# Kernel tuning notes

Hardware: AMD Instinct MI355X
Metric: run time of the kernel (lower is better)

The kernel has to match this reference:

```python
import jax, jax.numpy as jnp
import numpy as np

B, S, V, D, E, L = 4, 256, 50000, 300, 128, 20  # batch, seq, vocab, embed, encoder_size, labels


def _gru(x, h0, wih, whh, bih, bhh):
    """Unidirectional torch-style GRU. x: [B,S,Din], h0: [B,H]. Returns ([B,S,H], [B,H])."""
    gx = jnp.einsum('bsd,hd->bsh', x, wih) + bih  # precompute all input projections [B,S,3H]

    def step(h, gx_t):
        gh = h @ whh.T + bhh
        xr, xz, xn = jnp.split(gx_t, 3, axis=-1)
        hr, hz, hn = jnp.split(gh, 3, axis=-1)
        r = jax.nn.sigmoid(xr + hr)
        z = jax.nn.sigmoid(xz + hz)
        n = jnp.tanh(xn + r * hn)
        h2 = (1.0 - z) * n + z * h
        return h2, h2

    hT, hs = jax.lax.scan(step, h0, jnp.swapaxes(gx, 0, 1))
    return jnp.swapaxes(hs, 0, 1), hT


def _bigru(x, h0, pf, pb):
    """Bidirectional GRU. h0: [2,B,H]. Returns ([B,S,2H], [2,B,H])."""
    of, hf = _gru(x, h0[0], *pf)
    ob, hb = _gru(x[:, ::-1], h0[1], *pb)
    return jnp.concatenate([of, ob[:, ::-1]], axis=-1), jnp.stack([hf, hb])


def reference(inputs, emb,
              enc_wih_f, enc_whh_f, enc_bih_f, enc_bhh_f,
              enc_wih_b, enc_whh_b, enc_bih_b, enc_bhh_b,
              hid_wih_f, hid_whh_f, hid_bih_f, hid_bhh_f,
              hid_wih_b, hid_whh_b, hid_bih_b, hid_bhh_b,
              agg_wih_f, agg_whh_f, agg_bih_f, agg_bhh_f,
              agg_wih_b, agg_whh_b, agg_bih_b, agg_bhh_b,
              Wc1, Wc2, vc, Wb, Wd, vd, Wm, vm, Ws, vs, Wp, vp, Wpred):
    x = emb[inputs]                                # [B,S,D]
    b = x.shape[0]
    h0 = jnp.zeros((2, b, E), x.dtype)
    hp, hidden = _bigru(x, h0,
                        (enc_wih_f, enc_whh_f, enc_bih_f, enc_bhh_f),
                        (enc_wih_b, enc_whh_b, enc_bih_b, enc_bhh_b))   # [B,S,2E]
    hq, _ = _bigru(hp, hidden,
                   (hid_wih_f, hid_whh_f, hid_bih_f, hid_bhh_f),
                   (hid_wih_b, hid_whh_b, hid_bih_b, hid_bhh_b))        # [B,S,2E]

    # ptc: additive attention, score = vc . tanh(Wc1 hp_k + Wc2 hq_q)
    s1 = jnp.einsum('bkd,ed->bke', hp, Wc1)
    s2 = jnp.einsum('bqd,ed->bqe', hq, Wc2)
    sc = jnp.einsum('bqke,e->bqk', jnp.tanh(s1[:, None] + s2[:, :, None]), vc)
    ptc = jnp.einsum('bqk,bkd->bqd', jax.nn.softmax(sc, -1), hp)

    # ptb: bilinear attention, score = hq_q . (Wb hp_k)
    sc = jnp.einsum('bqd,bkd->bqk', hq, jnp.einsum('bkd,ed->bke', hp, Wb))
    ptb = jnp.einsum('bqk,bkd->bqd', jax.nn.softmax(sc, -1), hp)

    # ptd: score = vd . tanh(Wd (hp_k * hq_q))
    sc = jnp.einsum('bqke,e->bqk', jnp.tanh(jnp.einsum('bqkd,ed->bqke', hp[:, None] * hq[:, :, None], Wd)), vd)
    ptd = jnp.einsum('bqk,bkd->bqd', jax.nn.softmax(sc, -1), hp)

    # ptm: score = vm . tanh(Wm (hp_k - hq_q))
    sc = jnp.einsum('bqke,e->bqk', jnp.tanh(jnp.einsum('bqkd,ed->bqke', hp[:, None] - hq[:, :, None], Wm)), vm)
    ptm = jnp.einsum('bqk,bkd->bqd', jax.nn.softmax(sc, -1), hp)

    # pts: self, score = vs . tanh(Ws (hq_k * hq_q))
    sc = jnp.einsum('bqke,e->bqk', jnp.tanh(jnp.einsum('bqkd,ed->bqke', hq[:, None] * hq[:, :, None], Ws)), vs)
    pts = jnp.einsum('bqk,bkd->bqd', jax.nn.softmax(sc, -1), hq)

    agg = jnp.concatenate([hq, pts, ptc, ptd, ptb, ptm], axis=-1)  # [B,S,12E]
    agg_rep, _ = _bigru(agg, jnp.zeros((2, b, E), x.dtype),
                        (agg_wih_f, agg_whh_f, agg_bih_f, agg_bhh_f),
                        (agg_wih_b, agg_whh_b, agg_bih_b, agg_bhh_b))  # [B,S,2E]

    # pooled query rl over hq
    sj = jnp.einsum('bse,e->bs', jnp.tanh(jnp.einsum('bsd,ed->bse', hq, Wp)), vp)
    rl = jnp.einsum('bs,bsd->bd', jax.nn.softmax(sj, -1), hq)       # [B,2E]

    # final pooling over agg_rep (note: no tanh here, matching source)
    sc = jnp.einsum('bse,e->bs',
                    jnp.einsum('bsd,ed->bse', agg_rep, Wc1) + jnp.einsum('bd,ed->be', rl, Wc2)[:, None],
                    vc)
    rr = jnp.einsum('bs,bsd->bd', jax.nn.softmax(sc, -1), agg_rep)  # [B,2E]
    return jax.nn.sigmoid(rr @ Wpred.T)                              # [B,labels]


def setup_inputs() -> dict:
    key = jax.random.key(0)
    ks = iter(jax.random.split(key, 64))
    f = lambda *s: jax.random.normal(next(ks), s, jnp.float32) * 0.05
    H3 = 3 * E
    return dict(
        inputs=jax.random.randint(next(ks), (B, S), 0, V),
        emb=f(V, D),
        enc_wih_f=f(H3, D), enc_whh_f=f(H3, E), enc_bih_f=f(H3), enc_bhh_f=f(H3),
        enc_wih_b=f(H3, D), enc_whh_b=f(H3, E), enc_bih_b=f(H3), enc_bhh_b=f(H3),
        hid_wih_f=f(H3, 2 * E), hid_whh_f=f(H3, E), hid_bih_f=f(H3), hid_bhh_f=f(H3),
        hid_wih_b=f(H3, 2 * E), hid_whh_b=f(H3, E), hid_bih_b=f(H3), hid_bhh_b=f(H3),
        agg_wih_f=f(H3, 12 * E), agg_whh_f=f(H3, E), agg_bih_f=f(H3), agg_bhh_f=f(H3),
        agg_wih_b=f(H3, 12 * E), agg_whh_b=f(H3, E), agg_bih_b=f(H3), agg_bhh_b=f(H3),
        Wc1=f(E, 2 * E), Wc2=f(E, 2 * E), vc=f(E),
        Wb=f(2 * E, 2 * E),
        Wd=f(E, 2 * E), vd=f(E),
        Wm=f(E, 2 * E), vm=f(E),
        Ws=f(E, 2 * E), vs=f(E),
        Wp=f(E, 2 * E), vp=f(E),
        Wpred=f(L, 2 * E),
    )
```

## Files before the change

### kernel.cpp

```cpp
#include <hip/hip_runtime.h>
#include <math.h>

#define BB 4
#define SS 256
#define DD 300
#define DP 304
#define EE 128
#define LL 20
#define H3 384
#define D2 256
#define D12 1536

typedef __attribute__((ext_vector_type(8)))  short short8;
typedef __attribute__((ext_vector_type(16))) float f32x16;
typedef __attribute__((ext_vector_type(2)))  float f32x2;

__device__ __forceinline__ float tanh_fast(float x){
  float e = __expf(2.f*x);
  return 1.f - 2.f/(e+1.f);
}
__device__ __forceinline__ float sigmoidf_(float x){ return 1.f/(1.f+__expf(-x)); }
__device__ __forceinline__ float bf16_to_f(unsigned u){ return __builtin_bit_cast(float, u<<16); }
__device__ __forceinline__ float bf16hi_to_f(unsigned u){ return __builtin_bit_cast(float, u & 0xFFFF0000u); }
__device__ __forceinline__ unsigned bf16_rne(float f){
  unsigned u = __builtin_bit_cast(unsigned, f);
  return (u + 0x7FFFu + ((u>>16)&1u)) >> 16;
}
__device__ __forceinline__ unsigned pack_bf16x2(float lo, float hi){
  return bf16_rne(lo) | (bf16_rne(hi)<<16);
}

__global__ void k_cvt_bf16(const float* __restrict__ src, unsigned short* __restrict__ dst, int n2){
  int i = blockIdx.x*blockDim.x + threadIdx.x;
  if (i < n2){
    float2 f = *(const float2*)(src + 2*i);
    *(unsigned*)(dst + 2*i) = pack_bf16x2(f.x, f.y);
  }
}

struct CvtSeg { const float* src; unsigned short* dst; int rows, Ks, Kd; };
struct CvtArgs { CvtSeg s[13]; };
__global__ void k_cvt_weights(CvtArgs a){
  CvtSeg sg = a.s[blockIdx.y];
  int p = blockIdx.x*256 + threadIdx.x;
  int Kd2 = sg.Kd>>1;
  int npairs = sg.rows*Kd2;
  if (p >= npairs) return;
  int row = p/Kd2, kk = (p - row*Kd2)*2;
  float f0 = (kk   < sg.Ks)? sg.src[(size_t)row*sg.Ks+kk  ] : 0.f;
  float f1 = (kk+1 < sg.Ks)? sg.src[(size_t)row*sg.Ks+kk+1] : 0.f;
  *(unsigned*)(sg.dst + (size_t)row*sg.Kd + kk) = pack_bf16x2(f0,f1);
}

__global__ void k_embed(const int* __restrict__ inp, const float* __restrict__ emb,
                        unsigned short* __restrict__ xb){
  int row = blockIdx.x;
  int idx = inp[row];
  const float* src = emb + (size_t)idx*DD;
  unsigned short* dst = xb + (size_t)row*DP;
  int p = threadIdx.x;
  if (p < DP/2){
    float f0 = (2*p   < DD)? src[2*p  ] : 0.f;
    float f1 = (2*p+1 < DD)? src[2*p+1] : 0.f;
    *(unsigned*)(dst + 2*p) = pack_bf16x2(f0,f1);
  }
}

__global__ void k_init2(float* __restrict__ gf, const float* __restrict__ bf,
                        float* __restrict__ gb, const float* __restrict__ bb){
  int row = blockIdx.x, n = threadIdx.x;
  gf[(size_t)row*H3+n] = bf[n];
  gb[(size_t)row*H3+n] = bb[n];
}

__global__ __launch_bounds__(64) void k_mmbf(
    const unsigned short* __restrict__ X, const unsigned short* __restrict__ W,
    const float* __restrict__ bias, float* __restrict__ out,
    int N, int K, int kspan){
  int lane=threadIdx.x, col=lane&31, half=lane>>5;
  int n0=blockIdx.x*32, m0=blockIdx.y*64;
  int ks=blockIdx.z*kspan, ke=ks+kspan; if (ke>K) ke=K;
  const unsigned short* pa0 = X + (size_t)(m0+col)*K + half*8;
  const unsigned short* pa1 = pa0 + (size_t)32*K;
  const unsigned short* pb  = W + (size_t)(n0+col)*K + half*8;
  f32x16 acc0={}, acc1={};
  #pragma unroll 2
  for (int k=ks;k<ke;k+=16){
    short8 a0=__builtin_bit_cast(short8, *(const uint4*)(pa0+k));
    short8 a1=__builtin_bit_cast(short8, *(const uint4*)(pa1+k));
    short8 bv=__builtin_bit_cast(short8, *(const uint4*)(pb +k));
    acc0=__builtin_amdgcn_mfma_f32_32x32x16_bf16(a0,bv,acc0,0,0,0);
    acc1=__builtin_amdgcn_mfma_f32_32x32x16_bf16(a1,bv,acc1,0,0,0);
  }
  int cn = n0+col;
  if (gridDim.z==1){
    float bn = bias? bias[cn] : 0.f;
    #pragma unroll
    for (int r=0;r<16;r++){
      int row=(r&3)+8*(r>>2)+4*half;
      out[(size_t)(m0+row)*N+cn]    = acc0[r]+bn;
      out[(size_t)(m0+32+row)*N+cn] = acc1[r]+bn;
    }
  } else {
    #pragma unroll
    for (int r=0;r<16;r++){
      int row=(r&3)+8*(r>>2)+4*half;
      atomicAdd(&out[(size_t)(m0+row)*N+cn],    acc0[r]);
      atomicAdd(&out[(size_t)(m0+32+row)*N+cn], acc1[r]);
    }
  }
}

#define GW 8
#define CH 16
#define PSTR 9

__global__ __launch_bounds__(512, 1) void k_gru_scan(
                          const float* __restrict__ gxf, const float* __restrict__ gxb,
                          const float* __restrict__ whhf, const float* __restrict__ whhb,
                          const float* __restrict__ bhhf, const float* __restrict__ bhhb,
                          const float* __restrict__ h0,
                          float* __restrict__ out,
                          unsigned short* __restrict__ out_bf,
                          float* __restrict__ hT){
  int b=blockIdx.x, dir=blockIdx.y, tid=threadIdx.x;
  const float* gx  = dir? gxb : gxf;
  const float* whh = dir? whhb : whhf;
  const float* bhh = dir? bhhb : bhhf;
  int w = tid>>6, lane = tid&63;
  int chunk = w*CH;

  f32x2 wv[3][CH];
  #pragma unroll
  for (int p=0;p<3;p++){
    const float* r0 = whh + (size_t)(lane+64*(2*p  ))*EE + chunk;
    const float* r1 = whh + (size_t)(lane+64*(2*p+1))*EE + chunk;
    #pragma unroll
    for (int k=0;k<CH;k++){ wv[p][k].x = r0[k]; wv[p][k].y = r1[k]; }
  }

  __shared__ __align__(16) float hsh[EE];
  __shared__ float part[H3*PSTR];

  bool comb = (tid < EE);
  float hprev=0.f, b_r=0.f, b_z=0.f, b_n=0.f;
  float xrA=0.f,xzA=0.f,xnA=0.f, xrB=0.f,xzB=0.f,xnB=0.f;
  if (comb){
    int r = tid;
    b_r = bhh[r]; b_z = bhh[r+EE]; b_n = bhh[r+2*EE];
    hprev = h0? h0[((size_t)dir*BB+b)*EE + r] : 0.f;
    hsh[r] = hprev;
    int s0 = dir? (SS-1) : 0;
    int s1 = dir? (SS-2) : 1;
    const float* g0 = gx + ((size_t)b*SS+s0)*H3;
    const float* g1 = gx + ((size_t)b*SS+s1)*H3;
    xrA=g0[r]; xzA=g0[r+EE]; xnA=g0[r+2*EE];
    xrB=g1[r]; xzB=g1[r+EE]; xnB=g1[r+2*EE];
  }
  __syncthreads();

  auto dotphase = [&](){
    float vh = hsh[chunk + (lane & (CH-1))];
    f32x2 acc0={0.f,0.f}, acc1={0.f,0.f}, acc2={0.f,0.f};
    #pragma unroll
    for (int k=0;k<CH;k++){
      float s = __builtin_bit_cast(float,
                  __builtin_amdgcn_readlane(__builtin_bit_cast(int, vh), k));
      acc0 += wv[0][k]*s;
      acc1 += wv[1][k]*s;
      acc2 += wv[2][k]*s;
    }
    part[(lane      )*PSTR + w] = acc0.x;
    part[(lane+ 64  )*PSTR + w] = acc0.y;
    part[(lane+128  )*PSTR + w] = acc1.x;
    part[(lane+192  )*PSTR + w] = acc1.y;
    part[(lane+256  )*PSTR + w] = acc2.x;
    part[(lane+320  )*PSTR + w] = acc2.y;
  };

  auto combphase = [&](int t, float xr, float xz, float xn,
                       float& pxr, float& pxz, float& pxn){
    int r = tid;
    float ar=0.f, az=0.f, an=0.f;
    #pragma unroll
    for (int c=0;c<GW;c++){
      ar += part[(r      )*PSTR+c];
      az += part[(r+128  )*PSTR+c];
      an += part[(r+256  )*PSTR+c];
    }
    int s = dir? (SS-1-t) : t;
    float rg = sigmoidf_(xr + ar + b_r);
    float zg = sigmoidf_(xz + az + b_z);
    float ng = tanh_fast(xn + rg*(an + b_n));
    float h2 = (1.f-zg)*ng + zg*hprev;
    hprev = h2;
    hsh[r] = h2;
    size_t oi = ((size_t)b*SS+s)*D2 + (size_t)dir*EE + r;
    out[oi] = h2;
    if (out_bf) out_bf[oi] = (unsigned short)bf16_rne(h2);
    if (t+2 < SS){
      int sn = dir? (SS-3-t) : (t+2);
      const float* gn = gx + ((size_t)b*SS+sn)*H3;
      pxr=gn[r]; pxz=gn[r+EE]; pxn=gn[r+2*EE];
    }
  };

  for (int t=0;t<SS;t+=2){
    dotphase();
    __syncthreads();
    if (comb) combphase(t, xrA,xzA,xnA, xrA,xzA,xnA);
    __syncthreads();
    dotphase();
    __syncthreads();
    if (comb) combphase(t+1, xrB,xzB,xnB, xrB,xzB,xnB);
    __syncthreads();
  }
  if (hT && comb) hT[((size_t)dir*BB+b)*EE+tid]=hprev;
}

__global__ void k_copy_hq(const unsigned short* __restrict__ hqb, unsigned short* __restrict__ aggb){
  int row=blockIdx.x;
  aggb[(size_t)row*D12 + threadIdx.x] = hqb[(size_t)row*D2 + threadIdx.x];
}

__device__ __forceinline__ void softmax256(float val, float* red, float* p){
  int tid=threadIdx.x;
  red[tid]=val; __syncthreads();
  for (int st=128; st>0; st>>=1){ if (tid<st) red[tid]=fmaxf(red[tid],red[tid+st]); __syncthreads(); }
  float mx=red[0]; __syncthreads();
  float ex=__expf(val-mx); red[tid]=ex; __syncthreads();
  for (int st=128; st>0; st>>=1){ if (tid<st) red[tid]+=red[tid+st]; __syncthreads(); }
  float inv=1.f/red[0];
  p[tid]=ex*inv; __syncthreads();
}

__global__ __launch_bounds__(256) void k_attn_add(const float* __restrict__ A, const float* __restrict__ Bq,
                          const float* __restrict__ v, float sign,
                          const float* __restrict__ V, unsigned short* __restrict__ aggout, int off){
  __shared__ __align__(16) float bq[EE];
  __shared__ __align__(16) float vv[EE];
  __shared__ float p[SS]; __shared__ float red[SS];
  int q=blockIdx.x, b=blockIdx.y, tid=threadIdx.x;
  if (tid<EE){ bq[tid]=sign*Bq[((size_t)b*SS+q)*EE+tid]; vv[tid]=v[tid]; }
  __syncthreads();
  const float* Ar = A + ((size_t)b*SS+tid)*EE;
  float s=0.f;
  #pragma unroll
  for (int e=0;e<EE;e+=4){
    float4 a=*(const float4*)(Ar+e);
    float4 bb=*(const float4*)(bq+e);
    float4 vw=*(const float4*)(vv+e);
    s += vw.x*tanh_fast(a.x+bb.x)+vw.y*tanh_fast(a.y+bb.y)+vw.z*tanh_fast(a.z+bb.z)+vw.w*tanh_fast(a.w+bb.w);
  }
  softmax256(s, red, p);
  const float* V0 = V + (size_t)b*SS*D2;
  float o=0.f;
  for (int k=0;k<SS;k++) o += p[k]*V0[(size_t)k*D2+tid];
  aggout[((size_t)b*SS+q)*D12 + off + tid] = (unsigned short)bf16_rne(o);
}

__global__ __launch_bounds__(256) void k_attn_bil(const float* __restrict__ Pb, const float* __restrict__ hq,
                          const float* __restrict__ V, unsigned short* __restrict__ aggout, int off){
  __shared__ __align__(16) float hqq[D2];
  __shared__ float p[SS]; __shared__ float red[SS];
  int q=blockIdx.x, b=blockIdx.y, tid=threadIdx.x;
  hqq[tid]=hq[((size_t)b*SS+q)*D2+tid];
  __syncthreads();
  const float* Pr = Pb + ((size_t)b*SS+tid)*D2;
  float s=0.f;
  #pragma unroll
  for (int d=0;d<D2;d+=4){
    float4 a=*(const float4*)(Pr+d);
    float4 hh=*(const float4*)(hqq+d);
    s += a.x*hh.x+a.y*hh.y+a.z*hh.z+a.w*hh.w;
  }
  softmax256(s, red, p);
  const float* V0 = V + (size_t)b*SS*D2;
  float o=0.f;
  for (int k=0;k<SS;k++) o += p[k]*V0[(size_t)k*D2+tid];
  aggout[((size_t)b*SS+q)*D12 + off + tid] = (unsigned short)bf16_rne(o);
}

__global__ __launch_bounds__(256, 2) void k_mulattn_fused(
    const unsigned short* __restrict__ keysb,
    const float* __restrict__ qm,
    const unsigned short* __restrict__ Wb,
    const float* __restrict__ v,
    const float* __restrict__ V,
    unsigned short* __restrict__ aggout, int off){
  __shared__ __align__(16) float qrow[D2];
  __shared__ __align__(16) float vrow[EE];
  __shared__ float scq[SS];
  __shared__ float red[SS];
  __shared__ float p[SS];
  int q=blockIdx.x, b=blockIdx.y, tid=threadIdx.x;
  int wave=tid>>6, lane=tid&63;
  size_t bS = (size_t)b*SS;
  qrow[tid]=qm[(bS+q)*D2+tid];
  if (tid<EE) vrow[tid]=v[tid];
  __syncthreads();

  f32x16 acc[2][4]={};
  int m0 = wave*64;
  int col = lane&31, half = lane>>5;
  const unsigned short* krow0 = keysb + (bS + m0 + col)*D2 + half*8;
  const unsigned short* krow1 = krow0 + 32*D2;
  const unsigned short* wrow[4];
  #pragma unroll
  for (int n=0;n<4;n++) wrow[n] = Wb + (size_t)(n*32+col)*D2 + half*8;

  for (int d0=0; d0<D2; d0+=16){
    float4 qsA = *(const float4*)&qrow[d0 + half*8];
    float4 qsB = *(const float4*)&qrow[d0 + half*8 + 4];
    short8 bfrag[4];
    #pragma unroll
    for (int n=0;n<4;n++) bfrag[n] = __builtin_bit_cast(short8, *(const uint4*)(wrow[n]+d0));
    #pragma unroll
    for (int i=0;i<2;i++){
      uint4 raw = *(const uint4*)((i? krow1:krow0) + d0);
      float f0=bf16_to_f(raw.x)*qsA.x, f1=bf16hi_to_f(raw.x)*qsA.y;
      float f2=bf16_to_f(raw.y)*qsA.z, f3=bf16hi_to_f(raw.y)*qsA.w;
      float f4=bf16_to_f(raw.z)*qsB.x, f5=bf16hi_to_f(raw.z)*qsB.y;
      float f6=bf16_to_f(raw.w)*qsB.z, f7=bf16hi_to_f(raw.w)*qsB.w;
      uint4 pk;
      pk.x=pack_bf16x2(f0,f1);
      pk.y=pack_bf16x2(f2,f3);
      pk.z=pack_bf16x2(f4,f5);
      pk.w=pack_bf16x2(f6,f7);
      short8 afrag = __builtin_bit_cast(short8, pk);
      #pragma unroll
      for (int n=0;n<4;n++)
        acc[i][n] = __builtin_amdgcn_mfma_f32_32x32x16_bf16(afrag, bfrag[n], acc[i][n], 0,0,0);
    }
  }
  float vn[4];
  #pragma unroll
  for (int n=0;n<4;n++) vn[n]=vrow[n*32+col];
  #pragma unroll
  for (int i=0;i<2;i++){
    #pragma unroll
    for (int r=0;r<16;r++){
      float s = vn[0]*tanh_fast(acc[i][0][r]) + vn[1]*tanh_fast(acc[i][1][r])
              + vn[2]*tanh_fast(acc[i][2][r]) + vn[3]*tanh_fast(acc[i][3][r]);
      s += __shfl_xor(s,1,32); s += __shfl_xor(s,2,32); s += __shfl_xor(s,4,32);
      s += __shfl_xor(s,8,32); s += __shfl_xor(s,16,32);
      int k = m0 + i*32 + (r&3) + 8*(r>>2) + 4*half;
      scq[k] = s;
    }
  }
  __syncthreads();
  float val = scq[tid];
  softmax256(val, red, p);
  const float* V0 = V + bS*D2;
  float o=0.f;
  for (int k=0;k<SS;k++) o += p[k]*V0[(size_t)k*D2+tid];
  aggout[(bS+q)*D12 + off + tid] = (unsigned short)bf16_rne(o);
}

__global__ __launch_bounds__(256) void k_rl(const float* __restrict__ spj, const float* __restrict__ hq,
                    const float* __restrict__ vp, const float* __restrict__ Wc2,
                    float* __restrict__ sB){
  __shared__ __align__(16) float vpl[EE];
  __shared__ float p[SS]; __shared__ float red[SS];
  __shared__ __align__(16) float rr[D2];
  int b=blockIdx.x, tid=threadIdx.x;
  if (tid<EE) vpl[tid]=vp[tid];
  __syncthreads();
  const float* row = spj + ((size_t)b*SS+tid)*EE;
  float sj=0.f;
  #pragma unroll
  for (int e=0;e<EE;e+=4){
    float4 a=*(const float4*)(row+e);
    float4 vw=*(const float4*)(vpl+e);
    sj += vw.x*tanh_fast(a.x)+vw.y*tanh_fast(a.y)+vw.z*tanh_fast(a.z)+vw.w*tanh_fast(a.w);
  }
  softmax256(sj, red, p);
  float o=0.f;
  for (int s=0;s<SS;s++) o += p[s]*hq[((size_t)b*SS+s)*D2+tid];
  rr[tid]=o; __syncthreads();
  if (tid<EE){
    const float* wr = Wc2 + (size_t)tid*D2;
    float a=0.f;
    #pragma unroll
    for (int d=0;d<D2;d+=4){
      float4 w4=*(const float4*)(wr+d);
      float4 r4=*(const float4*)(rr+d);
      a += w4.x*r4.x+w4.y*r4.y+w4.z*r4.z+w4.w*r4.w;
    }
    sB[(size_t)b*EE+tid]=a;
  }
}

__global__ __launch_bounds__(256) void k_final(const float* __restrict__ sA, const float* __restrict__ sB,
                       const float* __restrict__ vc, const float* __restrict__ agg_rep,
                       const float* __restrict__ Wpred, float* __restrict__ out){
  __shared__ __align__(16) float sBl[EE];
  __shared__ __align__(16) float vcl[EE];
  __shared__ float p[SS]; __shared__ float red[SS]; __shared__ float rr[D2];
  int b=blockIdx.x, tid=threadIdx.x;
  if (tid<EE){ sBl[tid]=sB[(size_t)b*EE+tid]; vcl[tid]=vc[tid]; }
  __syncthreads();
  const float* rowA = sA + ((size_t)b*SS+tid)*EE;
  float sc=0.f;
  #pragma unroll
  for (int e=0;e<EE;e+=4){
    float4 a=*(const float4*)(rowA+e);
    float4 bb=*(const float4*)(sBl+e);
    float4 vw=*(const float4*)(vcl+e);
    sc += vw.x*(a.x+bb.x)+vw.y*(a.y+bb.y)+vw.z*(a.z+bb.z)+vw.w*(a.w+bb.w);
  }
  softmax256(sc, red, p);
  float o=0.f;
  for (int s=0;s<SS;s++) o += p[s]*agg_rep[((size_t)b*SS+s)*D2+tid];
  rr[tid]=o; __syncthreads();
  if (tid<LL){
    float a=0.f;
    const float* wr = Wpred + (size_t)tid*D2;
    for (int d=0;d<D2;d++) a += wr[d]*rr[d];
    out[(size_t)b*LL+tid]=sigmoidf_(a);
  }
}

extern "C" void kernel_launch(void* const* d_in, const int* in_sizes, int n_in,
                              void* d_out, int out_size, void* d_ws, size_t ws_size,
                              hipStream_t stream){
  (void)in_sizes; (void)n_in; (void)out_size; (void)ws_size;
  const int*   inp = (const int*)d_in[0];
  const float* emb = (const float*)d_in[1];
  const float* enc_wih_f=(const float*)d_in[2],  *enc_whh_f=(const float*)d_in[3],
             *enc_bih_f=(const float*)d_in[4],  *enc_bhh_f=(const float*)d_in[5];
  const float* enc_wih_b=(const float*)d_in[6],  *enc_whh_b=(const float*)d_in[7],
             *enc_bih_b=(const float*)d_in[8],  *enc_bhh_b=(const float*)d_in[9];
  const float* hid_wih_f=(const float*)d_in[10], *hid_whh_f=(const float*)d_in[11],
             *hid_bih_f=(const float*)d_in[12], *hid_bhh_f=(const float*)d_in[13];
  const float* hid_wih_b=(const float*)d_in[14], *hid_whh_b=(const float*)d_in[15],
             *hid_bih_b=(const float*)d_in[16], *hid_bhh_b=(const float*)d_in[17];
  const float* agg_wih_f=(const float*)d_in[18], *agg_whh_f=(const float*)d_in[19],
             *agg_bih_f=(const float*)d_in[20], *agg_bhh_f=(const float*)d_in[21];
  const float* agg_wih_b=(const float*)d_in[22], *agg_whh_b=(const float*)d_in[23],
             *agg_bih_b=(const float*)d_in[24], *agg_bhh_b=(const float*)d_in[25];
  const float* Wc1=(const float*)d_in[26], *Wc2=(const float*)d_in[27], *vc=(const float*)d_in[28];
  const float* Wb =(const float*)d_in[29];
  const float* Wd =(const float*)d_in[30], *vd=(const float*)d_in[31];
  const float* Wm =(const float*)d_in[32], *vm=(const float*)d_in[33];
  const float* Ws =(const float*)d_in[34], *vs=(const float*)d_in[35];
  const float* Wp =(const float*)d_in[36], *vp=(const float*)d_in[37];
  const float* Wpred=(const float*)d_in[38];

  float* ws = (float*)d_ws;
  size_t o = 0;
  float* gxf     = ws + o; o += (size_t)BB*SS*H3;
  float* gxb     = ws + o; o += (size_t)BB*SS*H3;
  float* hp      = ws + o; o += (size_t)BB*SS*D2;
  float* hq      = ws + o; o += (size_t)BB*SS*D2;
  float* hidden  = ws + o; o += (size_t)2*BB*EE;
  float* s1      = ws + o; o += (size_t)BB*SS*EE;
  float* s2      = ws + o; o += (size_t)BB*SS*EE;
  float* Am      = ws + o; o += (size_t)BB*SS*EE;
  float* Bm      = ws + o; o += (size_t)BB*SS*EE;
  float* Pb      = ws + o; o += (size_t)BB*SS*D2;
  float* spj     = ws + o; o += (size_t)BB*SS*EE;
  float* agg_rep = ws + o; o += (size_t)BB*SS*D2;
  float* sA      = ws + o; o += (size_t)BB*SS*EE;
  float* sB      = ws + o; o += (size_t)BB*EE;
  unsigned short* x_bf      = (unsigned short*)(ws+o); o += (size_t)BB*SS*DP/2;
  unsigned short* hp_bf     = (unsigned short*)(ws+o); o += (size_t)BB*SS*D2/2;
  unsigned short* hq_bf     = (unsigned short*)(ws+o); o += (size_t)BB*SS*D2/2;
  unsigned short* agg_bf    = (unsigned short*)(ws+o); o += (size_t)BB*SS*D12/2;
  unsigned short* aggrep_bf = (unsigned short*)(ws+o); o += (size_t)BB*SS*D2/2;
  unsigned short* encf_bf   = (unsigned short*)(ws+o); o += (size_t)H3*DP/2;
  unsigned short* encb_bf   = (unsigned short*)(ws+o); o += (size_t)H3*DP/2;
  unsigned short* hidf_bf   = (unsigned short*)(ws+o); o += (size_t)H3*D2/2;
  unsigned short* hidb_bf   = (unsigned short*)(ws+o); o += (size_t)H3*D2/2;
  unsigned short* aggf_bf   = (unsigned short*)(ws+o); o += (size_t)H3*D12/2;
  unsigned short* aggb_bf   = (unsigned short*)(ws+o); o += (size_t)H3*D12/2;
  unsigned short* Wc1_bf    = (unsigned short*)(ws+o); o += (size_t)EE*D2/2;
  unsigned short* Wc2_bf    = (unsigned short*)(ws+o); o += (size_t)EE*D2/2;
  unsigned short* Wm_bf     = (unsigned short*)(ws+o); o += (size_t)EE*D2/2;
  unsigned short* Wb_bf     = (unsigned short*)(ws+o); o += (size_t)D2*D2/2;
  unsigned short* Wp_bf     = (unsigned short*)(ws+o); o += (size_t)EE*D2/2;
  unsigned short* Wd_bf     = (unsigned short*)(ws+o); o += (size_t)EE*D2/2;
  unsigned short* Ws_bf     = (unsigned short*)(ws+o); o += (size_t)EE*D2/2;

  const int M = BB*SS;
  auto mmbf=[&](const unsigned short* X,const unsigned short* W,const float* bias,
                float* outp,int N,int K,int z,int kspan){
    dim3 g(N/32, M/64, z);
    k_mmbf<<<g,64,0,stream>>>(X,W,bias,outp,N,K,kspan);
  };

  k_embed<<<M,256,0,stream>>>(inp, emb, x_bf);
  CvtArgs ca;
  ca.s[0]  = {enc_wih_f, encf_bf, H3, DD, DP};
  ca.s[1]  = {enc_wih_b, encb_bf, H3, DD, DP};
  ca.s[2]  = {hid_wih_f, hidf_bf, H3, D2, D2};
  ca.s[3]  = {hid_wih_b, hidb_bf, H3, D2, D2};
  ca.s[4]  = {agg_wih_f, aggf_bf, H3, D12, D12};
  ca.s[5]  = {agg_wih_b, aggb_bf, H3, D12, D12};
  ca.s[6]  = {Wc1, Wc1_bf, EE, D2, D2};
  ca.s[7]  = {Wc2, Wc2_bf, EE, D2, D2};
  ca.s[8]  = {Wm,  Wm_bf,  EE, D2, D2};
  ca.s[9]  = {Wb,  Wb_bf,  D2, D2, D2};
  ca.s[10] = {Wp,  Wp_bf,  EE, D2, D2};
  ca.s[11] = {Wd,  Wd_bf,  EE, D2, D2};
  ca.s[12] = {Ws,  Ws_bf,  EE, D2, D2};
  {
    int maxpairs = H3*D12/2;
    dim3 g((maxpairs+255)/256, 13);
    k_cvt_weights<<<g,256,0,stream>>>(ca);
  }

  k_init2<<<M,H3,0,stream>>>(gxf, enc_bih_f, gxb, enc_bih_b);
  mmbf(x_bf, encf_bf, nullptr, gxf, H3, DP, 4, 80);
  mmbf(x_bf, encb_bf, nullptr, gxb, H3, DP, 4, 80);
  k_gru_scan<<<dim3(BB,2),512,0,stream>>>(gxf,gxb,enc_whh_f,enc_whh_b,enc_bhh_f,enc_bhh_b,
                                          nullptr,hp,hp_bf,hidden);

  k_init2<<<M,H3,0,stream>>>(gxf, hid_bih_f, gxb, hid_bih_b);
  mmbf(hp_bf, hidf_bf, nullptr, gxf, H3, D2, 4, 64);
  mmbf(hp_bf, hidb_bf, nullptr, gxb, H3, D2, 4, 64);
  k_gru_scan<<<dim3(BB,2),512,0,stream>>>(gxf,gxb,hid_whh_f,hid_whh_b,hid_bhh_f,hid_bhh_b,
                                          hidden,hq,hq_bf,nullptr);

  mmbf(hp_bf, Wc1_bf, nullptr, s1,  EE, D2, 1, D2);
  mmbf(hq_bf, Wc2_bf, nullptr, s2,  EE, D2, 1, D2);
  mmbf(hp_bf, Wm_bf,  nullptr, Am,  EE, D2, 1, D2);
  mmbf(hq_bf, Wm_bf,  nullptr, Bm,  EE, D2, 1, D2);
  mmbf(hp_bf, Wb_bf,  nullptr, Pb,  D2, D2, 1, D2);
  mmbf(hq_bf, Wp_bf,  nullptr, spj, EE, D2, 1, D2);

  k_copy_hq<<<M,256,0,stream>>>(hq_bf, agg_bf);
  dim3 gq(SS,BB);
  k_attn_add<<<gq,256,0,stream>>>(s1,s2,vc, 1.f, hp, agg_bf, 512);
  k_attn_add<<<gq,256,0,stream>>>(Am,Bm,vm,-1.f, hp, agg_bf, 1280);
  k_attn_bil<<<gq,256,0,stream>>>(Pb,hq,hp,agg_bf,1024);
  k_mulattn_fused<<<gq,256,0,stream>>>(hp_bf,hq,Wd_bf,vd,hp,agg_bf,768);
  k_mulattn_fused<<<gq,256,0,stream>>>(hq_bf,hq,Ws_bf,vs,hq,agg_bf,256);

  k_init2<<<M,H3,0,stream>>>(gxf, agg_bih_f, gxb, agg_bih_b);
  mmbf(agg_bf, aggf_bf, nullptr, gxf, H3, D12, 8, 192);
  mmbf(agg_bf, aggb_bf, nullptr, gxb, H3, D12, 8, 192);
  k_gru_scan<<<dim3(BB,2),512,0,stream>>>(gxf,gxb,agg_whh_f,agg_whh_b,agg_bhh_f,agg_bhh_b,
                                          nullptr,agg_rep,aggrep_bf,nullptr);

  k_rl<<<BB,256,0,stream>>>(spj,hq,vp,Wc2,sB);
  mmbf(aggrep_bf, Wc1_bf, nullptr, sA, EE, D2, 1, D2);
  k_final<<<BB,256,0,stream>>>(sA,sB,vc,agg_rep,Wpred,(float*)d_out);
}
```

Before: 1.126 ms.

## Fuse attention kernels, concatenate projection weights, drop split-K init and copy

Three attention heads (two additive and one bilinear) now run in one kernel that reads the shared value matrix once. The projection weights are concatenated so fewer, wider GEMMs produce s1/Am and s2/Bm/spj together. Split-K with atomics and the bias-init kernels are replaced by single-pass GEMMs that add the bias directly, and the GRU scan writes hq straight into the aggregation buffer. Softmax uses wave shuffle reductions instead of a shared-memory tree. The trade-off is lower GEMM grid parallelism without split-K, especially for K=1536.

```diff
diff --git a/kernel.cpp b/kernel.cpp
--- a/kernel.cpp
+++ b/kernel.cpp
@@ -30,16 +30,34 @@
   return bf16_rne(lo) | (bf16_rne(hi)<<16);
 }
 
-__global__ void k_cvt_bf16(const float* __restrict__ src, unsigned short* __restrict__ dst, int n2){
-  int i = blockIdx.x*blockDim.x + threadIdx.x;
-  if (i < n2){
-    float2 f = *(const float2*)(src + 2*i);
-    *(unsigned*)(dst + 2*i) = pack_bf16x2(f.x, f.y);
-  }
+__device__ __forceinline__ float wred_max(float v){
+  #pragma unroll
+  for (int st=1; st<64; st<<=1) v = fmaxf(v, __shfl_xor(v, st));
+  return v;
+}
+__device__ __forceinline__ float wred_sum(float v){
+  #pragma unroll
+  for (int st=1; st<64; st<<=1) v += __shfl_xor(v, st);
+  return v;
+}
+
+__device__ __forceinline__ void softmax256f(float val, float* red, float* p){
+  int tid=threadIdx.x, wv=tid>>6;
+  float m = wred_max(val);
+  if ((tid&63)==0) red[wv]=m;
+  __syncthreads();
+  float mx = fmaxf(fmaxf(red[0],red[1]),fmaxf(red[2],red[3]));
+  float ex = __expf(val-mx);
+  float s = wred_sum(ex);
+  if ((tid&63)==0) red[8+wv]=s;
+  __syncthreads();
+  float inv = 1.f/(red[8]+red[9]+red[10]+red[11]);
+  p[tid]=ex*inv;
+  __syncthreads();
 }
 
 struct CvtSeg { const float* src; unsigned short* dst; int rows, Ks, Kd; };
-struct CvtArgs { CvtSeg s[13]; };
+struct CvtArgs { CvtSeg s[14]; };
 __global__ void k_cvt_weights(CvtArgs a){
   CvtSeg sg = a.s[blockIdx.y];
   int p = blockIdx.x*256 + threadIdx.x;
@@ -64,13 +82,6 @@
     float f1 = (2*p+1 < DD)? src[2*p+1] : 0.f;
     *(unsigned*)(dst + 2*p) = pack_bf16x2(f0,f1);
   }
-}
-
-__global__ void k_init2(float* __restrict__ gf, const float* __restrict__ bf,
-                        float* __restrict__ gb, const float* __restrict__ bb){
-  int row = blockIdx.x, n = threadIdx.x;
-  gf[(size_t)row*H3+n] = bf[n];
-  gb[(size_t)row*H3+n] = bb[n];
 }
 
 __global__ __launch_bounds__(64) void k_mmbf(
@@ -122,6 +133,7 @@
                           const float* __restrict__ h0,
                           float* __restrict__ out,
                           unsigned short* __restrict__ out_bf,
+                          unsigned short* __restrict__ out_bf2,
                           float* __restrict__ hT){
   int b=blockIdx.x, dir=blockIdx.y, tid=threadIdx.x;
   const float* gx  = dir? gxb : gxf;
@@ -195,9 +207,12 @@
     float h2 = (1.f-zg)*ng + zg*hprev;
     hprev = h2;
     hsh[r] = h2;
-    size_t oi = ((size_t)b*SS+s)*D2 + (size_t)dir*EE + r;
+    size_t rowi = (size_t)b*SS+s;
+    size_t oi = rowi*D2 + (size_t)dir*EE + r;
     out[oi] = h2;
-    if (out_bf) out_bf[oi] = (unsigned short)bf16_rne(h2);
+    unsigned short hb = (unsigned short)bf16_rne(h2);
+    if (out_bf)  out_bf[oi] = hb;
+    if (out_bf2) out_bf2[rowi*D12 + (size_t)dir*EE + r] = hb;
     if (t+2 < SS){
       int sn = dir? (SS-3-t) : (t+2);
       const float* gn = gx + ((size_t)b*SS+sn)*H3;
@@ -218,67 +233,78 @@
   if (hT && comb) hT[((size_t)dir*BB+b)*EE+tid]=hprev;
 }
 
-__global__ void k_copy_hq(const unsigned short* __restrict__ hqb, unsigned short* __restrict__ aggb){
-  int row=blockIdx.x;
-  aggb[(size_t)row*D12 + threadIdx.x] = hqb[(size_t)row*D2 + threadIdx.x];
-}
-
-__device__ __forceinline__ void softmax256(float val, float* red, float* p){
-  int tid=threadIdx.x;
-  red[tid]=val; __syncthreads();
-  for (int st=128; st>0; st>>=1){ if (tid<st) red[tid]=fmaxf(red[tid],red[tid+st]); __syncthreads(); }
-  float mx=red[0]; __syncthreads();
-  float ex=__expf(val-mx); red[tid]=ex; __syncthreads();
-  for (int st=128; st>0; st>>=1){ if (tid<st) red[tid]+=red[tid+st]; __syncthreads(); }
-  float inv=1.f/red[0];
-  p[tid]=ex*inv; __syncthreads();
-}
-
-__global__ __launch_bounds__(256) void k_attn_add(const float* __restrict__ A, const float* __restrict__ Bq,
-                          const float* __restrict__ v, float sign,
-                          const float* __restrict__ V, unsigned short* __restrict__ aggout, int off){
+__global__ __launch_bounds__(256) void k_attn3(
+    const float* __restrict__ s1Am, const float* __restrict__ s2BS,
+    const float* __restrict__ Pb, const float* __restrict__ hq,
+    const float* __restrict__ vc, const float* __restrict__ vm,
+    const float* __restrict__ V, unsigned short* __restrict__ aggout){
   __shared__ __align__(16) float bq[EE];
-  __shared__ __align__(16) float vv[EE];
-  __shared__ float p[SS]; __shared__ float red[SS];
+  __shared__ __align__(16) float bm[EE];
+  __shared__ __align__(16) float vvc[EE];
+  __shared__ __align__(16) float vvm[EE];
+  __shared__ __align__(16) float hqq[D2];
+  __shared__ float pc[SS]; __shared__ float pm[SS]; __shared__ float pbl[SS];
+  __shared__ float red[32];
   int q=blockIdx.x, b=blockIdx.y, tid=threadIdx.x;
-  if (tid<EE){ bq[tid]=sign*Bq[((size_t)b*SS+q)*EE+tid]; vv[tid]=v[tid]; }
-  __syncthreads();
-  const float* Ar = A + ((size_t)b*SS+tid)*EE;
-  float s=0.f;
+  size_t bS=(size_t)b*SS;
+  if (tid<EE){
+    const float* qrow = s2BS + (bS+q)*384;
+    bq[tid]=qrow[tid]; bm[tid]=qrow[EE+tid];
+    vvc[tid]=vc[tid];  vvm[tid]=vm[tid];
+  }
+  hqq[tid]=hq[(bS+q)*D2+tid];
+  __syncthreads();
+
+  const float* kr = s1Am + (bS+tid)*(size_t)256;
+  float sc=0.f, sm=0.f;
   #pragma unroll
   for (int e=0;e<EE;e+=4){
-    float4 a=*(const float4*)(Ar+e);
-    float4 bb=*(const float4*)(bq+e);
-    float4 vw=*(const float4*)(vv+e);
-    s += vw.x*tanh_fast(a.x+bb.x)+vw.y*tanh_fast(a.y+bb.y)+vw.z*tanh_fast(a.z+bb.z)+vw.w*tanh_fast(a.w+bb.w);
-  }
-  softmax256(s, red, p);
-  const float* V0 = V + (size_t)b*SS*D2;
-  float o=0.f;
-  for (int k=0;k<SS;k++) o += p[k]*V0[(size_t)k*D2+tid];
-  aggout[((size_t)b*SS+q)*D12 + off + tid] = (unsigned short)bf16_rne(o);
-}
-
-__global__ __launch_bounds__(256) void k_attn_bil(const float* __restrict__ Pb, const float* __restrict__ hq,
-                          const float* __restrict__ V, unsigned short* __restrict__ aggout, int off){
-  __shared__ __align__(16) float hqq[D2];
-  __shared__ float p[SS]; __shared__ float red[SS];
-  int q=blockIdx.x, b=blockIdx.y, tid=threadIdx.x;
-  hqq[tid]=hq[((size_t)b*SS+q)*D2+tid];
-  __syncthreads();
-  const float* Pr = Pb + ((size_t)b*SS+tid)*D2;
-  float s=0.f;
+    float4 a1=*(const float4*)(kr+e);
+    float4 am=*(const float4*)(kr+EE+e);
+    float4 b1=*(const float4*)(bq+e);
+    float4 b2=*(const float4*)(bm+e);
+    float4 wc=*(const float4*)(vvc+e);
+    float4 wm=*(const float4*)(vvm+e);
+    sc += wc.x*tanh_fast(a1.x+b1.x)+wc.y*tanh_fast(a1.y+b1.y)
+        + wc.z*tanh_fast(a1.z+b1.z)+wc.w*tanh_fast(a1.w+b1.w);
+    sm += wm.x*tanh_fast(am.x-b2.x)+wm.y*tanh_fast(am.y-b2.y)
+        + wm.z*tanh_fast(am.z-b2.z)+wm.w*tanh_fast(am.w-b2.w);
+  }
+  float sb=0.f;
+  const float* Pr = Pb + (bS+tid)*(size_t)D2;
   #pragma unroll
   for (int d=0;d<D2;d+=4){
     float4 a=*(const float4*)(Pr+d);
     float4 hh=*(const float4*)(hqq+d);
-    s += a.x*hh.x+a.y*hh.y+a.z*hh.z+a.w*hh.w;
-  }
-  softmax256(s, red, p);
-  const float* V0 = V + (size_t)b*SS*D2;
-  float o=0.f;
-  for (int k=0;k<SS;k++) o += p[k]*V0[(size_t)k*D2+tid];
-  aggout[((size_t)b*SS+q)*D12 + off + tid] = (unsigned short)bf16_rne(o);
+    sb += a.x*hh.x+a.y*hh.y+a.z*hh.z+a.w*hh.w;
+  }
+
+  int wvid=tid>>6;
+  float m1=wred_max(sc), m2=wred_max(sm), m3=wred_max(sb);
+  if ((tid&63)==0){ red[wvid]=m1; red[4+wvid]=m2; red[8+wvid]=m3; }
+  __syncthreads();
+  m1=fmaxf(fmaxf(red[0],red[1]),fmaxf(red[2],red[3]));
+  m2=fmaxf(fmaxf(red[4],red[5]),fmaxf(red[6],red[7]));
+  m3=fmaxf(fmaxf(red[8],red[9]),fmaxf(red[10],red[11]));
+  float e1=__expf(sc-m1), e2=__expf(sm-m2), e3=__expf(sb-m3);
+  float t1=wred_sum(e1), t2=wred_sum(e2), t3=wred_sum(e3);
+  if ((tid&63)==0){ red[16+wvid]=t1; red[20+wvid]=t2; red[24+wvid]=t3; }
+  __syncthreads();
+  pc[tid] =e1/(red[16]+red[17]+red[18]+red[19]);
+  pm[tid] =e2/(red[20]+red[21]+red[22]+red[23]);
+  pbl[tid]=e3/(red[24]+red[25]+red[26]+red[27]);
+  __syncthreads();
+
+  const float* V0 = V + bS*D2;
+  float oc=0.f, om=0.f, ob=0.f;
+  for (int k=0;k<SS;k++){
+    float v=V0[(size_t)k*D2+tid];
+    oc+=pc[k]*v; om+=pm[k]*v; ob+=pbl[k]*v;
+  }
+  unsigned short* ao = aggout + (bS+q)*(size_t)D12;
+  ao[512 +tid]=(unsigned short)bf16_rne(oc);
+  ao[1280+tid]=(unsigned short)bf16_rne(om);
+  ao[1024+tid]=(unsigned short)bf16_rne(ob);
 }
 
 __global__ __launch_bounds__(256, 2) void k_mulattn_fused(
@@ -291,7 +317,7 @@
   __shared__ __align__(16) float qrow[D2];
   __shared__ __align__(16) float vrow[EE];
   __shared__ float scq[SS];
-  __shared__ float red[SS];
+  __shared__ float red[16];
   __shared__ float p[SS];
   int q=blockIdx.x, b=blockIdx.y, tid=threadIdx.x;
   int wave=tid>>6, lane=tid&63;
@@ -350,23 +376,23 @@
   }
   __syncthreads();
   float val = scq[tid];
-  softmax256(val, red, p);
+  softmax256f(val, red, p);
   const float* V0 = V + bS*D2;
   float o=0.f;
   for (int k=0;k<SS;k++) o += p[k]*V0[(size_t)k*D2+tid];
   aggout[(bS+q)*D12 + off + tid] = (unsigned short)bf16_rne(o);
 }
 
-__global__ __launch_bounds__(256) void k_rl(const float* __restrict__ spj, const float* __restrict__ hq,
+__global__ __launch_bounds__(256) void k_rl(const float* __restrict__ s2BS, const float* __restrict__ hq,
                     const float* __restrict__ vp, const float* __restrict__ Wc2,
                     float* __restrict__ sB){
   __shared__ __align__(16) float vpl[EE];
-  __shared__ float p[SS]; __shared__ float red[SS];
+  __shared__ float p[SS]; __shared__ float red[16];
   __shared__ __align__(16) float rr[D2];
   int b=blockIdx.x, tid=threadIdx.x;
   if (tid<EE) vpl[tid]=vp[tid];
   __syncthreads();
-  const float* row = spj + ((size_t)b*SS+tid)*EE;
+  const float* row = s2BS + ((size_t)b*SS+tid)*384 + 256;
   float sj=0.f;
   #pragma unroll
   for (int e=0;e<EE;e+=4){
@@ -374,7 +400,7 @@
     float4 vw=*(const float4*)(vpl+e);
     sj += vw.x*tanh_fast(a.x)+vw.y*tanh_fast(a.y)+vw.z*tanh_fast(a.z)+vw.w*tanh_fast(a.w);
   }
-  softmax256(sj, red, p);
+  softmax256f(sj, red, p);
   float o=0.f;
   for (int s=0;s<SS;s++) o += p[s]*hq[((size_t)b*SS+s)*D2+tid];
   rr[tid]=o; __syncthreads();
@@ -396,7 +422,7 @@
                        const float* __restrict__ Wpred, float* __restrict__ out){
   __shared__ __align__(16) float sBl[EE];
   __shared__ __align__(16) float vcl[EE];
-  __shared__ float p[SS]; __shared__ float red[SS]; __shared__ float rr[D2];
+  __shared__ float p[SS]; __shared__ float red[16]; __shared__ float rr[D2];
   int b=blockIdx.x, tid=threadIdx.x;
   if (tid<EE){ sBl[tid]=sB[(size_t)b*EE+tid]; vcl[tid]=vc[tid]; }
   __syncthreads();
@@ -409,7 +435,7 @@
     float4 vw=*(const float4*)(vcl+e);
     sc += vw.x*(a.x+bb.x)+vw.y*(a.y+bb.y)+vw.z*(a.z+bb.z)+vw.w*(a.w+bb.w);
   }
-  softmax256(sc, red, p);
+  softmax256f(sc, red, p);
   float o=0.f;
   for (int s=0;s<SS;s++) o += p[s]*agg_rep[((size_t)b*SS+s)*D2+tid];
   rr[tid]=o; __syncthreads();
@@ -454,12 +480,9 @@
   float* hp      = ws + o; o += (size_t)BB*SS*D2;
   float* hq      = ws + o; o += (size_t)BB*SS*D2;
   float* hidden  = ws + o; o += (size_t)2*BB*EE;
-  float* s1      = ws + o; o += (size_t)BB*SS*EE;
-  float* s2      = ws + o; o += (size_t)BB*SS*EE;
-  float* Am      = ws + o; o += (size_t)BB*SS*EE;
-  float* Bm      = ws + o; o += (size_t)BB*SS*EE;
+  float* s1Am    = ws + o; o += (size_t)BB*SS*256;
+  float* s2BS    = ws + o; o += (size_t)BB*SS*384;
   float* Pb      = ws + o; o += (size_t)BB*SS*D2;
-  float* spj     = ws + o; o += (size_t)BB*SS*EE;
   float* agg_rep = ws + o; o += (size_t)BB*SS*D2;
   float* sA      = ws + o; o += (size_t)BB*SS*EE;
   float* sB      = ws + o; o += (size_t)BB*EE;
@@ -474,19 +497,17 @@
   unsigned short* hidb_bf   = (unsigned short*)(ws+o); o += (size_t)H3*D2/2;
   unsigned short* aggf_bf   = (unsigned short*)(ws+o); o += (size_t)H3*D12/2;
   unsigned short* aggb_bf   = (unsigned short*)(ws+o); o += (size_t)H3*D12/2;
-  unsigned short* Wc1_bf    = (unsigned short*)(ws+o); o += (size_t)EE*D2/2;
-  unsigned short* Wc2_bf    = (unsigned short*)(ws+o); o += (size_t)EE*D2/2;
-  unsigned short* Wm_bf     = (unsigned short*)(ws+o); o += (size_t)EE*D2/2;
+  unsigned short* WA_bf     = (unsigned short*)(ws+o); o += (size_t)256*D2/2;
+  unsigned short* WB_bf     = (unsigned short*)(ws+o); o += (size_t)384*D2/2;
   unsigned short* Wb_bf     = (unsigned short*)(ws+o); o += (size_t)D2*D2/2;
-  unsigned short* Wp_bf     = (unsigned short*)(ws+o); o += (size_t)EE*D2/2;
   unsigned short* Wd_bf     = (unsigned short*)(ws+o); o += (size_t)EE*D2/2;
   unsigned short* Ws_bf     = (unsigned short*)(ws+o); o += (size_t)EE*D2/2;
 
   const int M = BB*SS;
   auto mmbf=[&](const unsigned short* X,const unsigned short* W,const float* bias,
-                float* outp,int N,int K,int z,int kspan){
-    dim3 g(N/32, M/64, z);
-    k_mmbf<<<g,64,0,stream>>>(X,W,bias,outp,N,K,kspan);
+                float* outp,int N,int K){
+    dim3 g(N/32, M/64, 1);
+    k_mmbf<<<g,64,0,stream>>>(X,W,bias,outp,N,K,K);
   };
 
   k_embed<<<M,256,0,stream>>>(inp, emb, x_bf);
@@ -497,53 +518,45 @@
   ca.s[3]  = {hid_wih_b, hidb_bf, H3, D2, D2};
   ca.s[4]  = {agg_wih_f, aggf_bf, H3, D12, D12};
   ca.s[5]  = {agg_wih_b, aggb_bf, H3, D12, D12};
-  ca.s[6]  = {Wc1, Wc1_bf, EE, D2, D2};
-  ca.s[7]  = {Wc2, Wc2_bf, EE, D2, D2};
-  ca.s[8]  = {Wm,  Wm_bf,  EE, D2, D2};
-  ca.s[9]  = {Wb,  Wb_bf,  D2, D2, D2};
-  ca.s[10] = {Wp,  Wp_bf,  EE, D2, D2};
-  ca.s[11] = {Wd,  Wd_bf,  EE, D2, D2};
-  ca.s[12] = {Ws,  Ws_bf,  EE, D2, D2};
+  ca.s[6]  = {Wc1, WA_bf,             EE, D2, D2};
+  ca.s[7]  = {Wm,  WA_bf + EE*D2,     EE, D2, D2};
+  ca.s[8]  = {Wc2, WB_bf,             EE, D2, D2};
+  ca.s[9]  = {Wm,  WB_bf + EE*D2,     EE, D2, D2};
+  ca.s[10] = {Wp,  WB_bf + 2*EE*D2,   EE, D2, D2};
+  ca.s[11] = {Wb,  Wb_bf, D2, D2, D2};
+  ca.s[12] = {Wd,  Wd_bf, EE, D2, D2};
+  ca.s[13] = {Ws,  Ws_bf, EE, D2, D2};
   {
     int maxpairs = H3*D12/2;
-    dim3 g((maxpairs+255)/256, 13);
+    dim3 g((maxpairs+255)/256, 14);
     k_cvt_weights<<<g,256,0,stream>>>(ca);
   }
 
-  k_init2<<<M,H3,0,stream>>>(gxf, enc_bih_f, gxb, enc_bih_b);
-  mmbf(x_bf, encf_bf, nullptr, gxf, H3, DP, 4, 80);
-  mmbf(x_bf, encb_bf, nullptr, gxb, H3, DP, 4, 80);
+  mmbf(x_bf, encf_bf, enc_bih_f, gxf, H3, DP);
+  mmbf(x_bf, encb_bf, enc_bih_b, gxb, H3, DP);
   k_gru_scan<<<dim3(BB,2),512,0,stream>>>(gxf,gxb,enc_whh_f,enc_whh_b,enc_bhh_f,enc_bhh_b,
-                                          nullptr,hp,hp_bf,hidden);
-
-  k_init2<<<M,H3,0,stream>>>(gxf, hid_bih_f, gxb, hid_bih_b);
-  mmbf(hp_bf, hidf_bf, nullptr, gxf, H3, D2, 4, 64);
-  mmbf(hp_bf, hidb_bf, nullptr, gxb, H3, D2, 4, 64);
+                                          nullptr,hp,hp_bf,nullptr,hidden);
+
+  mmbf(hp_bf, hidf_bf, hid_bih_f, gxf, H3, D2);
+  mmbf(hp_bf, hidb_bf, hid_bih_b, gxb, H3, D2);
   k_gru_scan<<<dim3(BB,2),512,0,stream>>>(gxf,gxb,hid_whh_f,hid_whh_b,hid_bhh_f,hid_bhh_b,
-                                          hidden,hq,hq_bf,nullptr);
-
-  mmbf(hp_bf, Wc1_bf, nullptr, s1,  EE, D2, 1, D2);
-  mmbf(hq_bf, Wc2_bf, nullptr, s2,  EE, D2, 1, D2);
-  mmbf(hp_bf, Wm_bf,  nullptr, Am,  EE, D2, 1, D2);
-  mmbf(hq_bf, Wm_bf,  nullptr, Bm,  EE, D2, 1, D2);
-  mmbf(hp_bf, Wb_bf,  nullptr, Pb,  D2, D2, 1, D2);
-  mmbf(hq_bf, Wp_bf,  nullptr, spj, EE, D2, 1, D2);
-
-  k_copy_hq<<<M,256,0,stream>>>(hq_bf, agg_bf);
+                                          hidden,hq,hq_bf,agg_bf,nullptr);
+
+  mmbf(hp_bf, WA_bf, nullptr, s1Am, 256, D2);
+  mmbf(hq_bf, WB_bf, nullptr, s2BS, 384, D2);
+  mmbf(hp_bf, Wb_bf, nullptr, Pb,   D2,  D2);
+
   dim3 gq(SS,BB);
-  k_attn_add<<<gq,256,0,stream>>>(s1,s2,vc, 1.f, hp, agg_bf, 512);
-  k_attn_add<<<gq,256,0,stream>>>(Am,Bm,vm,-1.f, hp, agg_bf, 1280);
-  k_attn_bil<<<gq,256,0,stream>>>(Pb,hq,hp,agg_bf,1024);
+  k_attn3<<<gq,256,0,stream>>>(s1Am, s2BS, Pb, hq, vc, vm, hp, agg_bf);
   k_mulattn_fused<<<gq,256,0,stream>>>(hp_bf,hq,Wd_bf,vd,hp,agg_bf,768);
   k_mulattn_fused<<<gq,256,0,stream>>>(hq_bf,hq,Ws_bf,vs,hq,agg_bf,256);
 
-  k_init2<<<M,H3,0,stream>>>(gxf, agg_bih_f, gxb, agg_bih_b);
-  mmbf(agg_bf, aggf_bf, nullptr, gxf, H3, D12, 8, 192);
-  mmbf(agg_bf, aggb_bf, nullptr, gxb, H3, D12, 8, 192);
+  mmbf(agg_bf, aggf_bf, agg_bih_f, gxf, H3, D12);
+  mmbf(agg_bf, aggb_bf, agg_bih_b, gxb, H3, D12);
   k_gru_scan<<<dim3(BB,2),512,0,stream>>>(gxf,gxb,agg_whh_f,agg_whh_b,agg_bhh_f,agg_bhh_b,
-                                          nullptr,agg_rep,aggrep_bf,nullptr);
-
-  k_rl<<<BB,256,0,stream>>>(spj,hq,vp,Wc2,sB);
-  mmbf(aggrep_bf, Wc1_bf, nullptr, sA, EE, D2, 1, D2);
+                                          nullptr,agg_rep,aggrep_bf,nullptr,nullptr);
+
+  k_rl<<<BB,256,0,stream>>>(s2BS,hq,vp,Wc2,sB);
+  mmbf(aggrep_bf, WA_bf, nullptr, sA, EE, D2);
   k_final<<<BB,256,0,stream>>>(sA,sB,vc,agg_rep,Wpred,(float*)d_out);
 }
```

After: 1.106 ms. Within noise of the previous version (-1.8%).
